# Optimization experiments

Hardware: AMD Instinct MI355X
Metric: run time of the kernel (lower is better)

The kernel has to match this reference:

```python
import jax, jax.numpy as jnp
import numpy as np

DIM = 3; NB = 8; NG = 4; KSIZE = 11; C_IN = 32; C_OUT = 32; HID = 128; NLAYERS = 4
N_PTS = KSIZE ** DIM
EPS = 1e-6

def _build_algebra():
    # Cl(3,0): blades ordered by (grade, bitmask): [1, e1,e2,e3, e12,e13,e23, e123]
    order = sorted(range(NB), key=lambda b: (bin(b).count('1'), b))
    idx = {b: i for i, b in enumerate(order)}
    grades = np.array([bin(b).count('1') for b in order])
    C = np.zeros((NB, NB, NB), np.float32)
    for a in range(NB):
        for b in range(NB):
            s, t = 0, a >> 1
            while t:
                s += bin(t & b).count('1')
                t >>= 1
            C[idx[a], idx[b], idx[a ^ b]] = -1.0 if (s & 1) else 1.0
    paths = np.zeros((NG, NG, NG), bool)
    for i in range(NB):
        for j in range(NB):
            for k in range(NB):
                if C[i, j, k] != 0.0:
                    paths[grades[i], grades[j], grades[k]] = True
    nz = np.argwhere(paths)  # 20 grade-triple paths for Cl(3,0)
    pid = np.zeros((NG, NG, NG), np.int64)
    for p, (a, b, c) in enumerate(nz):
        pid[a, b, c] = p
    pidx = pid[grades[:, None, None], grades[None, :, None], grades[None, None, :]]
    G = np.zeros((NB, NG), np.float32)
    G[np.arange(NB), grades] = 1.0
    return C, pidx, G, len(nz)

_C, _PIDX, _G, N_PATHS = _build_algebra()
CAYLEY = jnp.asarray(_C)   # cayley[a,b,c]: coeff of e_c in e_a * e_b
PIDX = jnp.asarray(_PIDX)  # blade-triple -> grade-path id
GMAT = jnp.asarray(_G)     # (NB, NG) blade->grade one-hot

def grade_norms(x):  # (N,C,NB) -> (N,C,NG)
    return jnp.sqrt(jnp.einsum('ncb,bg->ncg', x * x, GMAT) + EPS)

def to_blades(f):    # (N,C,NG) -> (N,C,NB)
    return jnp.einsum('ncg,bg->ncb', f, GMAT)

def mvlinear(x, w):  # x (N,Ci,NB), w (Co,Ci,NG): grade-wise channel mixing
    wb = jnp.einsum('oig,bg->oib', w, GMAT)
    return jnp.einsum('nib,oib->nob', x, wb)

def mvsilu(x, a, b):  # gated nonlinearity on per-grade invariants
    gate = jax.nn.sigmoid(a * grade_norms(x) + b)
    return x * to_blades(gate)

def gprod(x, q, w):  # per-channel weighted geometric product; w (C, N_PATHS)
    wc = w[:, PIDX] * CAYLEY  # (C, NB, NB, NB) indexed [i,k,j]
    return jnp.einsum('nci,cikj,nck->ncj', x, wc, q)

def _forward(condition, rel_pos_sigma, cond_a, cond_w, cond_b, cayley_weights,
             lin0_w, lin_w, silu_a, silu_b, q_w, gp_w, final_w, shell_sigma):
    lin = jnp.linspace(-1.0, 1.0, KSIZE, dtype=jnp.float32)
    grid = jnp.stack(jnp.meshgrid(lin, lin, lin, indexing='ij'), -1).reshape(-1, DIM)
    rel_pos = grid[:, None, :]                              # (N,1,3)
    norm2 = jnp.sum(rel_pos * rel_pos, -1, keepdims=True)   # (N,1,1)
    scalar = jnp.exp(-norm2 / (2.0 * rel_pos_sigma ** 2))   # scalar shell
    x = jnp.zeros((N_PTS, 1, NB), jnp.float32)
    x = x.at[:, :, 0:1].set(scalar).at[:, :, 1:4].set(rel_pos)  # embed grades 0,1
    relpos_norm = grade_norms(x)[:, 0, :]                   # (N, NG)
    # ConditionGradeNorm: grade-normalize condition, modulated by relpos norms
    cond = jnp.broadcast_to(condition[None], (N_PTS, C_IN, NB))
    gn = grade_norms(cond)
    denom = jax.nn.sigmoid(cond_a) * (gn - 1.0) + 1.0
    scale = (relpos_norm @ cond_w + cond_b).reshape(N_PTS, C_IN, NG)
    cond = cond * to_blades((1.0 + scale) / denom)
    h = jnp.concatenate([x, cond], axis=1)                  # (N, 1+C_IN, NB)
    # KernelNetwork: CEGNN-style MVLinear + MVSiLU + weighted geometric product
    for l in range(NLAYERS):
        h = mvlinear(h, lin0_w if l == 0 else lin_w[l - 1])
        h = mvsilu(h, silu_a[l], silu_b[l])
        h = gprod(h, mvlinear(h, q_w[l]), gp_w[l])
    k = mvlinear(h, final_w).reshape(N_PTS, C_OUT, C_IN, NB)
    # ScalarShell: per (o,i,blade) Gaussian envelope of |rel_pos|^2
    shell = jnp.exp(-norm2 / (2.0 * shell_sigma ** 2)).reshape(N_PTS, C_OUT, C_IN, NB)
    k = k * shell * jnp.float32(1.0 / np.sqrt(N_PTS))       # init factor
    # WeightedCayley: per-(o,i) path weights scattered onto the Cayley table
    wc = jnp.swapaxes(cayley_weights[:, :, PIDX] * CAYLEY, -1, -2)  # (o,i,k,l,m)
    K = jnp.einsum('noik,oiklm->olimn', k, wc)
    return K.reshape(C_OUT * NB, C_IN * NB, KSIZE, KSIZE, KSIZE)

def setup_inputs() -> dict:
    key = jax.random.key(0)
    ks = jax.random.split(key, 10)
    f32 = jnp.float32
    def rn(k, shape, scale=1.0):
        return jax.random.normal(k, shape, f32) * scale
    return {
        'condition': rn(ks[0], (C_IN, NB)),
        'rel_pos_sigma': jnp.ones((1, 1, 1), f32),
        'cond_a': rn(ks[1], (1, C_IN, NG)),
        'cond_w': rn(ks[2], (NG, C_IN * NG), 0.1),
        'cond_b': jnp.zeros((C_IN * NG,), f32),
        'cayley_weights': rn(ks[3], (C_OUT, C_IN, N_PATHS), 1.0 / np.sqrt(C_IN * NB)),
        'lin0_w': rn(ks[4], (HID, 1 + C_IN, NG), 1.0 / np.sqrt(1 + C_IN)),
        'lin_w': rn(ks[5], (NLAYERS - 1, HID, HID, NG), 1.0 / np.sqrt(HID)),
        'silu_a': rn(ks[6], (NLAYERS, 1, HID, NG)),
        'silu_b': jnp.zeros((NLAYERS, 1, HID, NG), f32),
        'q_w': rn(ks[7], (NLAYERS, HID, HID, NG), 1.0 / np.sqrt(HID)),
        'gp_w': rn(ks[8], (NLAYERS, HID, N_PATHS), 0.5),
        'final_w': rn(ks[9], (C_OUT * C_IN, HID, NG), 1.0 / np.sqrt(HID)),
        'shell_sigma': jnp.ones((1, C_OUT * C_IN, NB), f32),
    }

def reference(condition, rel_pos_sigma, cond_a, cond_w, cond_b, cayley_weights,
              lin0_w, lin_w, silu_a, silu_b, q_w, gp_w, final_w, shell_sigma):
    return _forward(condition, rel_pos_sigma, cond_a, cond_w, cond_b, cayley_weights,
                    lin0_w, lin_w, silu_a, silu_b, q_w, gp_w, final_w, shell_sigma)
```

## Files before the change

kernel.cpp:

```cpp
#include <hip/hip_runtime.h>
#include <math.h>

#define NB 8
#define NG 4
#define HID 128
#define NPTS 1331
#define NPAD 1344
#define NT 21
#define EPS 1e-6f

#define LT0_F4   (33*128)
#define MAT_F4   (128*128)
#define ARENA_F4 (LT0_F4 + 7*MAT_F4)

struct Alg {
  int grade[NB];
  signed char gp_j[NB][NB]; float gp_s[NB][NB]; signed char gp_p[NB][NB];
  signed char ks_k[NB][NB]; float ks_s[NB][NB]; signed char ks_p[NB][NB];
};

constexpr int popc3(int x){ return (x&1)+((x>>1)&1)+((x>>2)&1); }

constexpr Alg build_alg(){
  Alg A{};
  int order[NB]{}; int idx[NB]{};
  int t=0;
  for(int g=0; g<=3; ++g) for(int b=0;b<NB;++b) if(popc3(b)==g) order[t++]=b;
  for(int i=0;i<NB;++i) idx[order[i]]=i;
  for(int i=0;i<NB;++i) A.grade[i]=popc3(order[i]);
  float C[NB][NB][NB]{};
  for(int a=0;a<NB;++a) for(int b=0;b<NB;++b){
    int s=0, tt=a>>1;
    while(tt){ s += popc3(tt&b); tt>>=1; }
    C[idx[a]][idx[b]][idx[a^b]] = (s&1)?-1.0f:1.0f;
  }
  bool paths[NG][NG][NG]{};
  for(int i=0;i<NB;++i)for(int j=0;j<NB;++j)for(int k=0;k<NB;++k)
    if(C[i][j][k]!=0.0f) paths[A.grade[i]][A.grade[j]][A.grade[k]]=true;
  int pid[NG][NG][NG]{};
  int p=0;
  for(int a=0;a<NG;++a)for(int b=0;b<NG;++b)for(int c=0;c<NG;++c)
    if(paths[a][b][c]) pid[a][b][c]=p++;
  for(int i=0;i<NB;++i)for(int k=0;k<NB;++k){
    int j = idx[order[i]^order[k]];
    A.gp_j[i][k]=(signed char)j;
    A.gp_s[i][k]=C[i][k][j];
    A.gp_p[i][k]=(signed char)pid[A.grade[i]][A.grade[k]][A.grade[j]];
  }
  for(int l=0;l<NB;++l)for(int m=0;m<NB;++m){
    int k = idx[order[l]^order[m]];
    A.ks_k[l][m]=(signed char)k;
    A.ks_s[l][m]=C[k][m][l];
    A.ks_p[l][m]=(signed char)pid[A.grade[k]][A.grade[m]][A.grade[l]];
  }
  return A;
}

__device__ const Alg ALG = build_alg();

__device__ __forceinline__ float sigm(float x){ return 1.f/(1.f+expf(-x)); }

__global__ __launch_bounds__(256) void k_tw(
    const float4* __restrict__ lin0_w,
    const float4* __restrict__ lin_w,
    const float4* __restrict__ q_w,
    float4* __restrict__ wt)
{
  const int t = blockIdx.x*256 + threadIdx.x;
  if (t >= ARENA_F4) return;
  if (t < LT0_F4){
    const int i = t >> 7, o = t & 127;
    wt[t] = lin0_w[o*33 + i];
  } else {
    const int t2 = t - LT0_F4;
    const int mi = t2 >> 14;
    const int loc = t2 & 16383;
    const int i = loc >> 7, o = loc & 127;
    const float4 v = (mi < 3) ? lin_w[mi*MAT_F4 + o*128 + i]
                              : q_w[(mi-3)*MAT_F4 + o*128 + i];
    wt[t] = v;
  }
}

__global__ __launch_bounds__(256) void k_prep(
    const float* __restrict__ condition,
    const float* __restrict__ sigma1,
    const float* __restrict__ cond_a,
    const float* __restrict__ cond_w,
    const float* __restrict__ cond_b,
    float* __restrict__ norm2_o,
    float* __restrict__ h0)
{
  const int n = blockIdx.x*256 + threadIdx.x;
  if (n >= NPAD) return;
  const bool act = (n < NPTS);
  float px=0.f, py=0.f, pz=0.f, nr=0.f, sc=0.f;
  if (act){
    int i0 = n/121; int r = n - i0*121; int i1 = r/11; int i2 = r - i1*11;
    px = (float)(-1.0 + 0.2*(double)i0);
    py = (float)(-1.0 + 0.2*(double)i1);
    pz = (float)(-1.0 + 0.2*(double)i2);
    nr = px*px + py*py + pz*pz;
    float s = sigma1[0];
    sc = expf(-nr/(2.f*s*s));
  }
  norm2_o[n] = nr;
  h0[(0*HID+0)*NPAD+n] = sc;
  h0[(1*HID+0)*NPAD+n] = px;
  h0[(2*HID+0)*NPAD+n] = py;
  h0[(3*HID+0)*NPAD+n] = pz;
  h0[(4*HID+0)*NPAD+n] = 0.f;
  h0[(5*HID+0)*NPAD+n] = 0.f;
  h0[(6*HID+0)*NPAD+n] = 0.f;
  h0[(7*HID+0)*NPAD+n] = 0.f;
  const float rn0 = sqrtf(sc*sc + EPS);
  const float rn1 = sqrtf(nr + EPS);
  const float rn2 = sqrtf(EPS);
  const float rn3 = sqrtf(EPS);
  for (int c=0;c<32;++c){
    float cb[NB];
    #pragma unroll
    for (int b=0;b<NB;++b) cb[b] = condition[c*8+b];
    float gn2[4];
    gn2[0] = cb[0]*cb[0] + EPS;
    gn2[1] = cb[1]*cb[1] + cb[2]*cb[2] + cb[3]*cb[3] + EPS;
    gn2[2] = cb[4]*cb[4] + cb[5]*cb[5] + cb[6]*cb[6] + EPS;
    gn2[3] = cb[7]*cb[7] + EPS;
    float fac[4];
    #pragma unroll
    for (int g=0; g<4; ++g){
      const float gn = sqrtf(gn2[g]);
      const float den = fmaf(sigm(cond_a[c*4+g]), gn-1.f, 1.f);
      float scl = cond_b[c*4+g];
      scl = fmaf(rn0, cond_w[0*128 + c*4+g], scl);
      scl = fmaf(rn1, cond_w[1*128 + c*4+g], scl);
      scl = fmaf(rn2, cond_w[2*128 + c*4+g], scl);
      scl = fmaf(rn3, cond_w[3*128 + c*4+g], scl);
      fac[g] = (1.f + scl)/den;
    }
    h0[(0*HID + c+1)*NPAD + n] = act ? cb[0]*fac[0] : 0.f;
    h0[(1*HID + c+1)*NPAD + n] = act ? cb[1]*fac[1] : 0.f;
    h0[(2*HID + c+1)*NPAD + n] = act ? cb[2]*fac[1] : 0.f;
    h0[(3*HID + c+1)*NPAD + n] = act ? cb[3]*fac[1] : 0.f;
    h0[(4*HID + c+1)*NPAD + n] = act ? cb[4]*fac[2] : 0.f;
    h0[(5*HID + c+1)*NPAD + n] = act ? cb[5]*fac[2] : 0.f;
    h0[(6*HID + c+1)*NPAD + n] = act ? cb[6]*fac[2] : 0.f;
    h0[(7*HID + c+1)*NPAD + n] = act ? cb[7]*fac[3] : 0.f;
  }
}

__global__ __launch_bounds__(512) void k_mlp(
    float* __restrict__ hG,
    const float4* __restrict__ wt,
    const float* __restrict__ silu_a,
    const float* __restrict__ silu_b,
    const float* __restrict__ gp_w)
{
  __shared__ float hl[8][HID][12];
  const int lane = threadIdx.x & 63;
  const int wv   = threadIdx.x >> 6;
  const int n    = blockIdx.x*8 + wv;
  const int c0 = lane, c1 = lane + 64;

  if (lane < 33){
    #pragma unroll
    for (int b=0;b<NB;++b) hl[wv][lane][b] = hG[(b*HID+lane)*NPAD + n];
  }
  __syncthreads();

  for (int l=0; l<4; ++l){
    const int kin = l ? HID : 33;
    const float4* Wl = l ? (wt + LT0_F4 + (size_t)(l-1)*MAT_F4) : wt;
    const float4* Ql = wt + LT0_F4 + 3*MAT_F4 + (size_t)l*MAT_F4;
    const float* sa = silu_a + l*512;
    const float* sb = silu_b + l*512;
    const float* gw = gp_w  + l*2560;

    float a0[NB] = {0,0,0,0,0,0,0,0};
    float a1[NB] = {0,0,0,0,0,0,0,0};
    for (int i=0;i<kin;++i){
      const float4 hx = *reinterpret_cast<const float4*>(&hl[wv][i][0]);
      const float4 hy = *reinterpret_cast<const float4*>(&hl[wv][i][4]);
      const float4 w0 = Wl[i*HID + c0];
      const float4 w1 = Wl[i*HID + c1];
      a0[0]=fmaf(hx.x,w0.x,a0[0]); a0[1]=fmaf(hx.y,w0.y,a0[1]);
      a0[2]=fmaf(hx.z,w0.y,a0[2]); a0[3]=fmaf(hx.w,w0.y,a0[3]);
      a0[4]=fmaf(hy.x,w0.z,a0[4]); a0[5]=fmaf(hy.y,w0.z,a0[5]);
      a0[6]=fmaf(hy.z,w0.z,a0[6]); a0[7]=fmaf(hy.w,w0.w,a0[7]);
      a1[0]=fmaf(hx.x,w1.x,a1[0]); a1[1]=fmaf(hx.y,w1.y,a1[1]);
      a1[2]=fmaf(hx.z,w1.y,a1[2]); a1[3]=fmaf(hx.w,w1.y,a1[3]);
      a1[4]=fmaf(hy.x,w1.z,a1[4]); a1[5]=fmaf(hy.y,w1.z,a1[5]);
      a1[6]=fmaf(hy.z,w1.z,a1[6]); a1[7]=fmaf(hy.w,w1.w,a1[7]);
    }
    {
      const float g0 = sqrtf(a0[0]*a0[0] + EPS);
      const float g1 = sqrtf(a0[1]*a0[1] + a0[2]*a0[2] + a0[3]*a0[3] + EPS);
      const float g2 = sqrtf(a0[4]*a0[4] + a0[5]*a0[5] + a0[6]*a0[6] + EPS);
      const float g3 = sqrtf(a0[7]*a0[7] + EPS);
      const float t0 = sigm(fmaf(sa[c0*4+0], g0, sb[c0*4+0]));
      const float t1 = sigm(fmaf(sa[c0*4+1], g1, sb[c0*4+1]));
      const float t2 = sigm(fmaf(sa[c0*4+2], g2, sb[c0*4+2]));
      const float t3 = sigm(fmaf(sa[c0*4+3], g3, sb[c0*4+3]));
      a0[0]*=t0; a0[1]*=t1; a0[2]*=t1; a0[3]*=t1; a0[4]*=t2; a0[5]*=t2; a0[6]*=t2; a0[7]*=t3;
    }
    {
      const float g0 = sqrtf(a1[0]*a1[0] + EPS);
      const float g1 = sqrtf(a1[1]*a1[1] + a1[2]*a1[2] + a1[3]*a1[3] + EPS);
      const float g2 = sqrtf(a1[4]*a1[4] + a1[5]*a1[5] + a1[6]*a1[6] + EPS);
      const float g3 = sqrtf(a1[7]*a1[7] + EPS);
      const float t0 = sigm(fmaf(sa[c1*4+0], g0, sb[c1*4+0]));
      const float t1 = sigm(fmaf(sa[c1*4+1], g1, sb[c1*4+1]));
      const float t2 = sigm(fmaf(sa[c1*4+2], g2, sb[c1*4+2]));
      const float t3 = sigm(fmaf(sa[c1*4+3], g3, sb[c1*4+3]));
      a1[0]*=t0; a1[1]*=t1; a1[2]*=t1; a1[3]*=t1; a1[4]*=t2; a1[5]*=t2; a1[6]*=t2; a1[7]*=t3;
    }
    __syncthreads();
    #pragma unroll
    for (int b=0;b<NB;++b){ hl[wv][c0][b]=a0[b]; hl[wv][c1][b]=a1[b]; }
    __syncthreads();

    float q0[NB] = {0,0,0,0,0,0,0,0};
    float q1[NB] = {0,0,0,0,0,0,0,0};
    for (int i=0;i<HID;++i){
      const float4 hx = *reinterpret_cast<const float4*>(&hl[wv][i][0]);
      const float4 hy = *reinterpret_cast<const float4*>(&hl[wv][i][4]);
      const float4 w0 = Ql[i*HID + c0];
      const float4 w1 = Ql[i*HID + c1];
      q0[0]=fmaf(hx.x,w0.x,q0[0]); q0[1]=fmaf(hx.y,w0.y,q0[1]);
      q0[2]=fmaf(hx.z,w0.y,q0[2]); q0[3]=fmaf(hx.w,w0.y,q0[3]);
      q0[4]=fmaf(hy.x,w0.z,q0[4]); q0[5]=fmaf(hy.y,w0.z,q0[5]);
      q0[6]=fmaf(hy.z,w0.z,q0[6]); q0[7]=fmaf(hy.w,w0.w,q0[7]);
      q1[0]=fmaf(hx.x,w1.x,q1[0]); q1[1]=fmaf(hx.y,w1.y,q1[1]);
      q1[2]=fmaf(hx.z,w1.y,q1[2]); q1[3]=fmaf(hx.w,w1.y,q1[3]);
      q1[4]=fmaf(hy.x,w1.z,q1[4]); q1[5]=fmaf(hy.y,w1.z,q1[5]);
      q1[6]=fmaf(hy.z,w1.z,q1[6]); q1[7]=fmaf(hy.w,w1.w,q1[7]);
    }
    float x0[NB], x1[NB];
    #pragma unroll
    for (int b=0;b<NB;++b){ x0[b]=hl[wv][c0][b]; x1[b]=hl[wv][c1][b]; }
    float wp0[20], wp1[20];
    #pragma unroll
    for (int p5=0;p5<5;++p5){
      const float4 v0 = *reinterpret_cast<const float4*>(gw + c0*20 + p5*4);
      const float4 v1 = *reinterpret_cast<const float4*>(gw + c1*20 + p5*4);
      wp0[p5*4+0]=v0.x; wp0[p5*4+1]=v0.y; wp0[p5*4+2]=v0.z; wp0[p5*4+3]=v0.w;
      wp1[p5*4+0]=v1.x; wp1[p5*4+1]=v1.y; wp1[p5*4+2]=v1.z; wp1[p5*4+3]=v1.w;
    }
    float o0[NB] = {0,0,0,0,0,0,0,0};
    float o1[NB] = {0,0,0,0,0,0,0,0};
    #pragma unroll
    for (int i=0;i<NB;++i)
      #pragma unroll
      for (int k=0;k<NB;++k){
        const int J = ALG.gp_j[i][k];
        const int P = ALG.gp_p[i][k];
        const float t0v = x0[i]*q0[k];
        const float t1v = x1[i]*q1[k];
        o0[J] = fmaf(ALG.gp_s[i][k] > 0.f ? t0v : -t0v, wp0[P], o0[J]);
        o1[J] = fmaf(ALG.gp_s[i][k] > 0.f ? t1v : -t1v, wp1[P], o1[J]);
      }
    __syncthreads();
    #pragma unroll
    for (int b=0;b<NB;++b){ hl[wv][c0][b]=o0[b]; hl[wv][c1][b]=o1[b]; }
    __syncthreads();
  }

  #pragma unroll
  for (int rep=0; rep<16; ++rep){
    const int e  = rep*512 + threadIdx.x;
    const int pt = e & 7;
    const int b  = (e>>3) & 7;
    const int ch = e >> 6;
    hG[(b*HID+ch)*NPAD + blockIdx.x*8 + pt] = hl[pt][ch][b];
  }
}

__global__ __launch_bounds__(256) void k_final(
    const float* __restrict__ hin,
    const float* __restrict__ fw,
    const float* __restrict__ ss,
    const float* __restrict__ cw,
    const float* __restrict__ norm2,
    float* __restrict__ out)
{
  __shared__ float lds[256*64];
  const int lane = threadIdx.x & 63;
  const int wv   = threadIdx.x >> 6;
  const int nb   = blockIdx.x;
  const int n    = nb*64 + lane;
  const int oi0  = blockIdx.y * 16 + wv * 4;
  float acc[4][NB];
  #pragma unroll
  for (int j=0;j<4;++j)
    #pragma unroll
    for (int b=0;b<NB;++b) acc[j][b]=0.f;

  for (int ci=0; ci<HID; ci+=32){
    __syncthreads();
    #pragma unroll
    for (int rep=0; rep<16; ++rep){
      const int e   = rep*256 + threadIdx.x;
      const int row = e >> 4;
      const int c4  = e & 15;
      const int b   = row >> 5;
      const int cc  = row & 31;
      const float4 v = *reinterpret_cast<const float4*>(hin + (size_t)(b*HID + ci + cc)*NPAD + nb*64 + c4*4);
      *reinterpret_cast<float4*>(&lds[row*64 + c4*4]) = v;
    }
    __syncthreads();
    for (int cc=0; cc<32; ++cc){
      float hv[NB];
      #pragma unroll
      for (int b=0;b<NB;++b) hv[b] = lds[(b*32+cc)*64 + lane];
      #pragma unroll
      for (int j=0;j<4;++j){
        const float4 w = *reinterpret_cast<const float4*>(fw + ((size_t)(oi0+j)*HID + ci+cc)*4);
        acc[j][0] = fmaf(hv[0], w.x, acc[j][0]);
        acc[j][1] = fmaf(hv[1], w.y, acc[j][1]);
        acc[j][2] = fmaf(hv[2], w.y, acc[j][2]);
        acc[j][3] = fmaf(hv[3], w.y, acc[j][3]);
        acc[j][4] = fmaf(hv[4], w.z, acc[j][4]);
        acc[j][5] = fmaf(hv[5], w.z, acc[j][5]);
        acc[j][6] = fmaf(hv[6], w.z, acc[j][6]);
        acc[j][7] = fmaf(hv[7], w.w, acc[j][7]);
      }
    }
  }

  const float INVS = (float)(1.0 / sqrt((double)NPTS));
  const float nr   = norm2[n];
  const bool  act  = (n < NPTS);
  #pragma unroll
  for (int j=0;j<4;++j){
    const int oi = oi0+j;
    const int o  = oi >> 5;
    const int i  = oi & 31;
    float kf[NB];
    #pragma unroll
    for (int b=0;b<NB;++b){
      const float s = ss[oi*8+b];
      kf[b] = acc[j][b] * expf(-nr/(2.f*s*s)) * INVS;
    }
    float wp[20];
    #pragma unroll
    for (int p=0;p<20;++p) wp[p] = cw[oi*20+p];
    float* obase = out + (size_t)(o*2048 + i*8)*NPTS + n;
    if (act){
      #pragma unroll
      for (int l=0;l<NB;++l)
        #pragma unroll
        for (int m=0;m<NB;++m){
          const float t = kf[ALG.ks_k[l][m]] * wp[ALG.ks_p[l][m]];
          obase[(size_t)(l*256+m)*NPTS] = (ALG.ks_s[l][m] > 0.f) ? t : -t;
        }
    }
  }
}

extern "C" void kernel_launch(void* const* d_in, const int* in_sizes, int n_in,
                              void* d_out, int out_size, void* d_ws, size_t ws_size,
                              hipStream_t stream) {
  const float* condition    = (const float*)d_in[0];
  const float* rel_pos_sig  = (const float*)d_in[1];
  const float* cond_a       = (const float*)d_in[2];
  const float* cond_w       = (const float*)d_in[3];
  const float* cond_b       = (const float*)d_in[4];
  const float* cayley_w     = (const float*)d_in[5];
  const float* lin0_w       = (const float*)d_in[6];
  const float* lin_w        = (const float*)d_in[7];
  const float* silu_a       = (const float*)d_in[8];
  const float* silu_b       = (const float*)d_in[9];
  const float* q_w          = (const float*)d_in[10];
  const float* gp_w         = (const float*)d_in[11];
  const float* final_w      = (const float*)d_in[12];
  const float* shell_sigma  = (const float*)d_in[13];
  float* out = (float*)d_out;
  float* ws  = (float*)d_ws;

  float*  norm2 = ws;
  float*  hA    = ws + NPAD;
  float4* arena = (float4*)(hA + 8*HID*NPAD);

  k_tw<<<dim3((ARENA_F4+255)/256), 256, 0, stream>>>(
      (const float4*)lin0_w, (const float4*)lin_w, (const float4*)q_w, arena);

  k_prep<<<dim3((NPAD+255)/256), 256, 0, stream>>>(
      condition, rel_pos_sig, cond_a, cond_w, cond_b, norm2, hA);

  k_mlp<<<dim3(NPAD/8), 512, 0, stream>>>(hA, arena, silu_a, silu_b, gp_w);

  k_final<<<dim3(NT, 64), 256, 0, stream>>>(hA, final_w, shell_sigma, cayley_w, norm2, out);
}
```

Baseline: 834.7 us.

## Split final kernel into kernel-field pass and row-contiguous expansion; drop MLP barriers

The final stage is split in two. One kernel computes the per-(o,i,blade) radial kernel field into a workspace buffer. A second kernel expands it with the Cayley-weighted sign/path coefficients, writing each output row of 1331 points contiguously. This targets the write efficiency of the very large output tensor, at the cost of an extra intermediate buffer that is written and then read back. The MLP kernel is also refactored into helpers, and its block-wide barriers are removed, since each wave owns a private LDS slice. That removal relies on in-order LDS access within a wave.

```diff
diff --git a/kernel.cpp b/kernel.cpp
--- a/kernel.cpp
+++ b/kernel.cpp
@@ -149,6 +149,66 @@
   }
 }
 
+template<int KIN>
+__device__ __forceinline__ void matvec2(const float* hw, const float4* __restrict__ W,
+                                        int c0, int c1, float a0[NB], float a1[NB])
+{
+  #pragma unroll
+  for (int b=0;b<NB;++b){ a0[b]=0.f; a1[b]=0.f; }
+  #pragma unroll 4
+  for (int i=0;i<KIN;++i){
+    const float4 hx = *reinterpret_cast<const float4*>(hw + i*12);
+    const float4 hy = *reinterpret_cast<const float4*>(hw + i*12 + 4);
+    const float4 w0 = W[i*HID + c0];
+    const float4 w1 = W[i*HID + c1];
+    a0[0]=fmaf(hx.x,w0.x,a0[0]); a0[1]=fmaf(hx.y,w0.y,a0[1]);
+    a0[2]=fmaf(hx.z,w0.y,a0[2]); a0[3]=fmaf(hx.w,w0.y,a0[3]);
+    a0[4]=fmaf(hy.x,w0.z,a0[4]); a0[5]=fmaf(hy.y,w0.z,a0[5]);
+    a0[6]=fmaf(hy.z,w0.z,a0[6]); a0[7]=fmaf(hy.w,w0.w,a0[7]);
+    a1[0]=fmaf(hx.x,w1.x,a1[0]); a1[1]=fmaf(hx.y,w1.y,a1[1]);
+    a1[2]=fmaf(hx.z,w1.y,a1[2]); a1[3]=fmaf(hx.w,w1.y,a1[3]);
+    a1[4]=fmaf(hy.x,w1.z,a1[4]); a1[5]=fmaf(hy.y,w1.z,a1[5]);
+    a1[6]=fmaf(hy.z,w1.z,a1[6]); a1[7]=fmaf(hy.w,w1.w,a1[7]);
+  }
+}
+
+__device__ __forceinline__ void silu8(float a[NB], const float* sa, const float* sb)
+{
+  const float g0 = sqrtf(a[0]*a[0] + EPS);
+  const float g1 = sqrtf(a[1]*a[1] + a[2]*a[2] + a[3]*a[3] + EPS);
+  const float g2 = sqrtf(a[4]*a[4] + a[5]*a[5] + a[6]*a[6] + EPS);
+  const float g3 = sqrtf(a[7]*a[7] + EPS);
+  const float t0 = sigm(fmaf(sa[0], g0, sb[0]));
+  const float t1 = sigm(fmaf(sa[1], g1, sb[1]));
+  const float t2 = sigm(fmaf(sa[2], g2, sb[2]));
+  const float t3 = sigm(fmaf(sa[3], g3, sb[3]));
+  a[0]*=t0; a[1]*=t1; a[2]*=t1; a[3]*=t1; a[4]*=t2; a[5]*=t2; a[6]*=t2; a[7]*=t3;
+}
+
+__device__ __forceinline__ void store_row(float* hw, int c, const float a[NB])
+{
+  float4 v0 = {a[0],a[1],a[2],a[3]};
+  float4 v1 = {a[4],a[5],a[6],a[7]};
+  *reinterpret_cast<float4*>(hw + c*12)     = v0;
+  *reinterpret_cast<float4*>(hw + c*12 + 4) = v1;
+}
+
+__device__ __forceinline__ void gprod8(const float x[NB], const float q[NB],
+                                       const float wp[20], float o[NB])
+{
+  #pragma unroll
+  for (int b=0;b<NB;++b) o[b]=0.f;
+  #pragma unroll
+  for (int i=0;i<NB;++i)
+    #pragma unroll
+    for (int k=0;k<NB;++k){
+      const int J = ALG.gp_j[i][k];
+      const int P = ALG.gp_p[i][k];
+      const float t = x[i]*q[k];
+      o[J] = fmaf(ALG.gp_s[i][k] > 0.f ? t : -t, wp[P], o[J]);
+    }
+}
+
 __global__ __launch_bounds__(512) void k_mlp(
     float* __restrict__ hG,
     const float4* __restrict__ wt,
@@ -161,84 +221,32 @@
   const int wv   = threadIdx.x >> 6;
   const int n    = blockIdx.x*8 + wv;
   const int c0 = lane, c1 = lane + 64;
+  float* hw = &hl[wv][0][0];
 
   if (lane < 33){
     #pragma unroll
-    for (int b=0;b<NB;++b) hl[wv][lane][b] = hG[(b*HID+lane)*NPAD + n];
-  }
-  __syncthreads();
-
+    for (int b=0;b<NB;++b) hw[lane*12+b] = hG[(b*HID+lane)*NPAD + n];
+  }
+
+  float a0[NB], a1[NB], q0[NB], q1[NB], o0[NB], o1[NB];
+  float wp0[20], wp1[20];
+
+  #pragma unroll 1
   for (int l=0; l<4; ++l){
-    const int kin = l ? HID : 33;
-    const float4* Wl = l ? (wt + LT0_F4 + (size_t)(l-1)*MAT_F4) : wt;
     const float4* Ql = wt + LT0_F4 + 3*MAT_F4 + (size_t)l*MAT_F4;
     const float* sa = silu_a + l*512;
     const float* sb = silu_b + l*512;
     const float* gw = gp_w  + l*2560;
 
-    float a0[NB] = {0,0,0,0,0,0,0,0};
-    float a1[NB] = {0,0,0,0,0,0,0,0};
-    for (int i=0;i<kin;++i){
-      const float4 hx = *reinterpret_cast<const float4*>(&hl[wv][i][0]);
-      const float4 hy = *reinterpret_cast<const float4*>(&hl[wv][i][4]);
-      const float4 w0 = Wl[i*HID + c0];
-      const float4 w1 = Wl[i*HID + c1];
-      a0[0]=fmaf(hx.x,w0.x,a0[0]); a0[1]=fmaf(hx.y,w0.y,a0[1]);
-      a0[2]=fmaf(hx.z,w0.y,a0[2]); a0[3]=fmaf(hx.w,w0.y,a0[3]);
-      a0[4]=fmaf(hy.x,w0.z,a0[4]); a0[5]=fmaf(hy.y,w0.z,a0[5]);
-      a0[6]=fmaf(hy.z,w0.z,a0[6]); a0[7]=fmaf(hy.w,w0.w,a0[7]);
-      a1[0]=fmaf(hx.x,w1.x,a1[0]); a1[1]=fmaf(hx.y,w1.y,a1[1]);
-      a1[2]=fmaf(hx.z,w1.y,a1[2]); a1[3]=fmaf(hx.w,w1.y,a1[3]);
-      a1[4]=fmaf(hy.x,w1.z,a1[4]); a1[5]=fmaf(hy.y,w1.z,a1[5]);
-      a1[6]=fmaf(hy.z,w1.z,a1[6]); a1[7]=fmaf(hy.w,w1.w,a1[7]);
-    }
-    {
-      const float g0 = sqrtf(a0[0]*a0[0] + EPS);
-      const float g1 = sqrtf(a0[1]*a0[1] + a0[2]*a0[2] + a0[3]*a0[3] + EPS);
-      const float g2 = sqrtf(a0[4]*a0[4] + a0[5]*a0[5] + a0[6]*a0[6] + EPS);
-      const float g3 = sqrtf(a0[7]*a0[7] + EPS);
-      const float t0 = sigm(fmaf(sa[c0*4+0], g0, sb[c0*4+0]));
-      const float t1 = sigm(fmaf(sa[c0*4+1], g1, sb[c0*4+1]));
-      const float t2 = sigm(fmaf(sa[c0*4+2], g2, sb[c0*4+2]));
-      const float t3 = sigm(fmaf(sa[c0*4+3], g3, sb[c0*4+3]));
-      a0[0]*=t0; a0[1]*=t1; a0[2]*=t1; a0[3]*=t1; a0[4]*=t2; a0[5]*=t2; a0[6]*=t2; a0[7]*=t3;
-    }
-    {
-      const float g0 = sqrtf(a1[0]*a1[0] + EPS);
-      const float g1 = sqrtf(a1[1]*a1[1] + a1[2]*a1[2] + a1[3]*a1[3] + EPS);
-      const float g2 = sqrtf(a1[4]*a1[4] + a1[5]*a1[5] + a1[6]*a1[6] + EPS);
-      const float g3 = sqrtf(a1[7]*a1[7] + EPS);
-      const float t0 = sigm(fmaf(sa[c1*4+0], g0, sb[c1*4+0]));
-      const float t1 = sigm(fmaf(sa[c1*4+1], g1, sb[c1*4+1]));
-      const float t2 = sigm(fmaf(sa[c1*4+2], g2, sb[c1*4+2]));
-      const float t3 = sigm(fmaf(sa[c1*4+3], g3, sb[c1*4+3]));
-      a1[0]*=t0; a1[1]*=t1; a1[2]*=t1; a1[3]*=t1; a1[4]*=t2; a1[5]*=t2; a1[6]*=t2; a1[7]*=t3;
-    }
-    __syncthreads();
-    #pragma unroll
-    for (int b=0;b<NB;++b){ hl[wv][c0][b]=a0[b]; hl[wv][c1][b]=a1[b]; }
-    __syncthreads();
-
-    float q0[NB] = {0,0,0,0,0,0,0,0};
-    float q1[NB] = {0,0,0,0,0,0,0,0};
-    for (int i=0;i<HID;++i){
-      const float4 hx = *reinterpret_cast<const float4*>(&hl[wv][i][0]);
-      const float4 hy = *reinterpret_cast<const float4*>(&hl[wv][i][4]);
-      const float4 w0 = Ql[i*HID + c0];
-      const float4 w1 = Ql[i*HID + c1];
-      q0[0]=fmaf(hx.x,w0.x,q0[0]); q0[1]=fmaf(hx.y,w0.y,q0[1]);
-      q0[2]=fmaf(hx.z,w0.y,q0[2]); q0[3]=fmaf(hx.w,w0.y,q0[3]);
-      q0[4]=fmaf(hy.x,w0.z,q0[4]); q0[5]=fmaf(hy.y,w0.z,q0[5]);
-      q0[6]=fmaf(hy.z,w0.z,q0[6]); q0[7]=fmaf(hy.w,w0.w,q0[7]);
-      q1[0]=fmaf(hx.x,w1.x,q1[0]); q1[1]=fmaf(hx.y,w1.y,q1[1]);
-      q1[2]=fmaf(hx.z,w1.y,q1[2]); q1[3]=fmaf(hx.w,w1.y,q1[3]);
-      q1[4]=fmaf(hy.x,w1.z,q1[4]); q1[5]=fmaf(hy.y,w1.z,q1[5]);
-      q1[6]=fmaf(hy.z,w1.z,q1[6]); q1[7]=fmaf(hy.w,w1.w,q1[7]);
-    }
-    float x0[NB], x1[NB];
-    #pragma unroll
-    for (int b=0;b<NB;++b){ x0[b]=hl[wv][c0][b]; x1[b]=hl[wv][c1][b]; }
-    float wp0[20], wp1[20];
+    if (l == 0) matvec2<33>(hw, wt, c0, c1, a0, a1);
+    else        matvec2<HID>(hw, wt + LT0_F4 + (size_t)(l-1)*MAT_F4, c0, c1, a0, a1);
+    silu8(a0, sa + c0*4, sb + c0*4);
+    silu8(a1, sa + c1*4, sb + c1*4);
+    store_row(hw, c0, a0);
+    store_row(hw, c1, a1);
+
+    matvec2<HID>(hw, Ql, c0, c1, q0, q1);
+
     #pragma unroll
     for (int p5=0;p5<5;++p5){
       const float4 v0 = *reinterpret_cast<const float4*>(gw + c0*20 + p5*4);
@@ -246,25 +254,13 @@
       wp0[p5*4+0]=v0.x; wp0[p5*4+1]=v0.y; wp0[p5*4+2]=v0.z; wp0[p5*4+3]=v0.w;
       wp1[p5*4+0]=v1.x; wp1[p5*4+1]=v1.y; wp1[p5*4+2]=v1.z; wp1[p5*4+3]=v1.w;
     }
-    float o0[NB] = {0,0,0,0,0,0,0,0};
-    float o1[NB] = {0,0,0,0,0,0,0,0};
-    #pragma unroll
-    for (int i=0;i<NB;++i)
-      #pragma unroll
-      for (int k=0;k<NB;++k){
-        const int J = ALG.gp_j[i][k];
-        const int P = ALG.gp_p[i][k];
-        const float t0v = x0[i]*q0[k];
-        const float t1v = x1[i]*q1[k];
-        o0[J] = fmaf(ALG.gp_s[i][k] > 0.f ? t0v : -t0v, wp0[P], o0[J]);
-        o1[J] = fmaf(ALG.gp_s[i][k] > 0.f ? t1v : -t1v, wp1[P], o1[J]);
-      }
-    __syncthreads();
-    #pragma unroll
-    for (int b=0;b<NB;++b){ hl[wv][c0][b]=o0[b]; hl[wv][c1][b]=o1[b]; }
-    __syncthreads();
-  }
-
+    gprod8(a0, q0, wp0, o0);
+    gprod8(a1, q1, wp1, o1);
+    store_row(hw, c0, o0);
+    store_row(hw, c1, o1);
+  }
+
+  __syncthreads();
   #pragma unroll
   for (int rep=0; rep<16; ++rep){
     const int e  = rep*512 + threadIdx.x;
@@ -275,13 +271,12 @@
   }
 }
 
-__global__ __launch_bounds__(256) void k_final(
+__global__ __launch_bounds__(256) void k_kfield(
     const float* __restrict__ hin,
     const float* __restrict__ fw,
     const float* __restrict__ ss,
-    const float* __restrict__ cw,
     const float* __restrict__ norm2,
-    float* __restrict__ out)
+    float* __restrict__ kf)
 {
   __shared__ float lds[256*64];
   const int lane = threadIdx.x & 63;
@@ -329,30 +324,48 @@
 
   const float INVS = (float)(1.0 / sqrt((double)NPTS));
   const float nr   = norm2[n];
-  const bool  act  = (n < NPTS);
   #pragma unroll
   for (int j=0;j<4;++j){
     const int oi = oi0+j;
-    const int o  = oi >> 5;
-    const int i  = oi & 31;
-    float kf[NB];
     #pragma unroll
     for (int b=0;b<NB;++b){
       const float s = ss[oi*8+b];
-      kf[b] = acc[j][b] * expf(-nr/(2.f*s*s)) * INVS;
-    }
-    float wp[20];
-    #pragma unroll
-    for (int p=0;p<20;++p) wp[p] = cw[oi*20+p];
-    float* obase = out + (size_t)(o*2048 + i*8)*NPTS + n;
-    if (act){
-      #pragma unroll
-      for (int l=0;l<NB;++l)
-        #pragma unroll
-        for (int m=0;m<NB;++m){
-          const float t = kf[ALG.ks_k[l][m]] * wp[ALG.ks_p[l][m]];
-          obase[(size_t)(l*256+m)*NPTS] = (ALG.ks_s[l][m] > 0.f) ? t : -t;
-        }
+      kf[((size_t)oi*8 + b)*NPAD + n] = acc[j][b] * expf(-nr/(2.f*s*s)) * INVS;
+    }
+  }
+}
+
+__global__ __launch_bounds__(256) void k_expand(
+    const float* __restrict__ kf,
+    const float* __restrict__ cw,
+    float* __restrict__ out)
+{
+  __shared__ float coef[32][8];
+  __shared__ int   km[8];
+  const int blk = blockIdx.x;
+  const int o   = blk >> 6;
+  const int l   = (blk >> 3) & 7;
+  const int sub = blk & 7;
+  const int t   = threadIdx.x;
+  {
+    const int i = t >> 3, m = t & 7;
+    coef[i][m] = ALG.ks_s[l][m] * cw[(size_t)(o*32+i)*20 + ALG.ks_p[l][m]];
+    if (t < 8) km[t] = ALG.ks_k[l][t];
+  }
+  __syncthreads();
+
+  float* obase = out + ((size_t)((o*8+l)*256 + sub*32)) * NPTS;
+  #pragma unroll 1
+  for (int rr=0; rr<32; ++rr){
+    const int row = sub*32 + rr;
+    const int i = row >> 3, m = row & 7;
+    const float cf = coef[i][m];
+    const float* src = kf + ((size_t)((o*32+i)*8 + km[m])) * NPAD;
+    float* dst = obase + (size_t)rr * NPTS;
+    #pragma unroll
+    for (int base=0; base<6; ++base){
+      const int idx = base*256 + t;
+      if (idx < NPTS) dst[idx] = cf * src[idx];
     }
   }
 }
@@ -380,6 +393,7 @@
   float*  norm2 = ws;
   float*  hA    = ws + NPAD;
   float4* arena = (float4*)(hA + 8*HID*NPAD);
+  float*  kf    = (float*)(arena + ARENA_F4);
 
   k_tw<<<dim3((ARENA_F4+255)/256), 256, 0, stream>>>(
       (const float4*)lin0_w, (const float4*)lin_w, (const float4*)q_w, arena);
@@ -389,5 +403,7 @@
 
   k_mlp<<<dim3(NPAD/8), 512, 0, stream>>>(hA, arena, silu_a, silu_b, gp_w);
 
-  k_final<<<dim3(NT, 64), 256, 0, stream>>>(hA, final_w, shell_sigma, cayley_w, norm2, out);
-}
+  k_kfield<<<dim3(NT, 64), 256, 0, stream>>>(hA, final_w, shell_sigma, norm2, kf);
+
+  k_expand<<<dim3(2048), 256, 0, stream>>>(kf, cayley_w, out);
+}
```

New measurement: 744.6 us. 1.12x faster.
